# Kernel tuning notes

Measured on AMD Instinct MI355X. Metric: run time of the kernel, lower is better.

Reference implementation:

```python
import jax, jax.numpy as jnp
import numpy as np

# ---- module hyperparameters (from init_kwargs / tracker defaults) ----
D_MODEL = 512
D_HEAD = 512
LAMBDA_0 = 1.0        # A_0 = I / lambda_0
FIXED_LAMBDA = 1.0    # fixed penalty magnitude -> U = sqrt(lambda) * K (then / sqrt(d_head))
STAB_EPS = 1e-6       # InversePenaltyTracker.stabilization_eps
PERIODIC_EPS = 1e-6   # InversePenaltyTracker.periodic_eps
PERIOD = 128          # InversePenaltyTracker.period (periodic re-regularization)
EXPLODE_EPS = 1e-5    # fallback_add_explode coefficient
NORM_THRESH = 1000.0  # explosion detection threshold on Frobenius norms


def setup_inputs() -> dict:
    key = jax.random.key(0)
    ks = jax.random.split(key, 9)
    B, T, d = 8, 2048, D_MODEL
    s = 1.0 / np.sqrt(d)
    f32 = jnp.float32
    return {
        "x": jax.random.normal(ks[0], (B, T, d), f32),
        "Wq": (jax.random.normal(ks[1], (D_HEAD, d), f32) * s),
        "bq": jax.random.normal(ks[2], (D_HEAD,), f32) * 0.02,
        "Wk": (jax.random.normal(ks[3], (D_HEAD, d), f32) * s),
        "bk": jax.random.normal(ks[4], (D_HEAD,), f32) * 0.02,
        "Wv": (jax.random.normal(ks[5], (D_HEAD, d), f32) * s),
        "bv": jax.random.normal(ks[6], (D_HEAD,), f32) * 0.02,
        "Wo": (jax.random.normal(ks[7], (d, D_HEAD), f32) * s),
        "bo": jax.random.normal(ks[8], (d,), f32) * 0.02,
    }


def _vla_forward(x, Wq, bq, Wk, bk, Wv, bv, Wo, bo):
    B, T, _ = x.shape
    d = D_HEAD
    # projections (nn.Linear: x @ W.T + b)
    Q = jnp.einsum('btd,hd->bth', x, Wq) + bq
    K = jnp.einsum('btd,hd->bth', x, Wk) + bk
    V = jnp.einsum('btd,hd->bth', x, Wv) + bv

    # PenaltyBuilder (rank 1, fixed lambda): u_t = sqrt(lambda) * k_t, then / sqrt(d_head)
    U = (jnp.sqrt(jnp.float32(FIXED_LAMBDA)) / jnp.sqrt(jnp.float32(d))) * K
    s_seq = jnp.sum(K * Q, axis=-1)                                   # (B,T)
    Vn = V / (jnp.linalg.norm(V, axis=-1, keepdims=True) + 1e-6)      # (B,T,d)

    I = jnp.eye(d, dtype=jnp.float32)
    A0 = jnp.zeros((B, d, d), jnp.float32) + I / LAMBDA_0
    S0 = jnp.zeros((B, d, d), jnp.float32)

    def step(carry, inp):
        A, S = carry
        q, u, s_t, vn, t = inp  # q,u,vn: (B,d); s_t: (B,); t: scalar int
        # Sherman-Morrison rank-1 inverse update with stabilization
        z = jnp.einsum('bij,bj->bi', A, u)
        dot = jnp.sum(u * z, axis=-1)
        delta = jnp.maximum(1.0 + dot, 1e-6)
        unstable = (jnp.abs(delta) < STAB_EPS) | ~jnp.isfinite(delta)
        safe = jnp.where(unstable, 1.0, delta)
        upd = (z[:, :, None] * z[:, None, :]) / safe[:, None, None]
        A = jnp.where(unstable[:, None, None], A + STAB_EPS * I, A - upd)
        # periodic re-regularization (inv_step = t+1)
        A = jnp.where(((t + 1) % PERIOD) == 0, A + PERIODIC_EPS * I, A)
        # alpha_t = s_t * (A u_t)
        z2 = jnp.einsum('bij,bj->bi', A, u)
        alpha = s_t[:, None] * z2
        # memory update S += v_norm alpha^T
        S = S + vn[:, :, None] * alpha[:, None, :]
        # explosion guard
        Sn = jnp.linalg.norm(S.reshape(S.shape[0], -1), axis=-1)
        An = jnp.linalg.norm(A.reshape(A.shape[0], -1), axis=-1)
        A = jnp.where(((Sn > NORM_THRESH) | (An > NORM_THRESH))[:, None, None],
                      A + EXPLODE_EPS * I, A)
        o = jnp.einsum('bij,bj->bi', S, q)
        return (A, S), o

    xs = (jnp.swapaxes(Q, 0, 1), jnp.swapaxes(U, 0, 1),
          jnp.swapaxes(s_seq, 0, 1), jnp.swapaxes(Vn, 0, 1),
          jnp.arange(T))
    _, O = jax.lax.scan(step, (A0, S0), xs)    # O: (T,B,d)
    O = jnp.swapaxes(O, 0, 1)                  # (B,T,d)
    return jnp.einsum('bth,dh->btd', O, Wo) + bo


def reference(x, Wq, bq, Wk, bk, Wv, bv, Wo, bo):
    return _vla_forward(x, Wq, bq, Wk, bk, Wv, bv, Wo, bo)
```

## Files before the change

kernel.cpp:

```cpp
#include <hip/hip_runtime.h>
#include <hip/hip_bf16.h>

#define BB 8
#define TT 2048
#define DD 512
#define LL 128
#define NC 16
#define ETH 512

typedef unsigned short u16;
typedef unsigned int u32;
typedef __attribute__((ext_vector_type(8))) short bf16x8v;
typedef __attribute__((ext_vector_type(4))) float f32x4v;

__device__ __forceinline__ float bf2f(u32 h) { return __uint_as_float(h << 16); }
__device__ __forceinline__ u16 f2bf(float f) {
    u32 u = __float_as_uint(f);
    u += 0x7fffu + ((u >> 16) & 1u);
    return (u16)(u >> 16);
}
__device__ __forceinline__ float wred64(float v) {
    #pragma unroll
    for (int off = 32; off; off >>= 1) v += __shfl_xor(v, off);
    return v;
}
__device__ __forceinline__ void unpack8(uint4 r, float* f) {
    f[0] = bf2f(r.x & 0xffff); f[1] = bf2f(r.x >> 16);
    f[2] = bf2f(r.y & 0xffff); f[3] = bf2f(r.y >> 16);
    f[4] = bf2f(r.z & 0xffff); f[5] = bf2f(r.z >> 16);
    f[6] = bf2f(r.w & 0xffff); f[7] = bf2f(r.w >> 16);
}

__global__ __launch_bounds__(256)
void f2bf_kernel(const float4* __restrict__ in, ushort4* __restrict__ out, const int n4)
{
    int i = blockIdx.x * 256 + threadIdx.x;
    const int stride = gridDim.x * 256;
    for (; i < n4; i += stride) {
        const float4 v = in[i];
        ushort4 o;
        o.x = f2bf(v.x); o.y = f2bf(v.y); o.z = f2bf(v.z); o.w = f2bf(v.w);
        out[i] = o;
    }
}

__global__ __launch_bounds__(256)
void wconv_kernel(const float4* __restrict__ Wq, const float4* __restrict__ Wk,
                  const float4* __restrict__ Wv, const float4* __restrict__ Wo,
                  ushort4* __restrict__ oq, ushort4* __restrict__ ok,
                  ushort4* __restrict__ ov, ushort4* __restrict__ oo)
{
    const int i = blockIdx.x * 256 + threadIdx.x;
    const int y = blockIdx.y;
    const float4* src = (y == 0) ? Wq : (y == 1) ? Wk : (y == 2) ? Wv : Wo;
    ushort4* dst = (y == 0) ? oq : (y == 1) ? ok : (y == 2) ? ov : oo;
    const float4 v = src[i];
    ushort4 o;
    o.x = f2bf(v.x); o.y = f2bf(v.y); o.z = f2bf(v.z); o.w = f2bf(v.w);
    dst[i] = o;
}

template<int OUT_BF>
__global__ __launch_bounds__(256)
void mfma_gemm(const u16* __restrict__ Abf, const u16* __restrict__ Bbf,
               const float* __restrict__ bias, void* __restrict__ Cout,
               const float outscale)
{
    __shared__ u16 Asm[128 * 64];
    __shared__ u16 Bsm[128 * 64];
    const int tid = threadIdx.x;
    const int wave = tid >> 6, lane = tid & 63;
    const int wm = wave >> 1, wn = wave & 1;
    const int m0 = blockIdx.x * 128, n0 = blockIdx.y * 128;

    f32x4v acc[4][4];
    #pragma unroll
    for (int i = 0; i < 4; ++i)
        #pragma unroll
        for (int j = 0; j < 4; ++j)
            acc[i][j] = (f32x4v){0.f, 0.f, 0.f, 0.f};

    const u16* gsrcA[4];
    const u16* gsrcB[4];
    #pragma unroll
    for (int i = 0; i < 4; ++i) {
        const int idx = i * 256 + tid;
        const int row = idx >> 3, c = idx & 7;
        const int kb = c ^ (row & 7);
        gsrcA[i] = Abf + (size_t)(m0 + row) * 512 + kb * 8;
        gsrcB[i] = Bbf + (size_t)(n0 + row) * 512 + kb * 8;
    }

    for (int k0 = 0; k0 < 512; k0 += 64) {
        __syncthreads();
        #pragma unroll
        for (int i = 0; i < 4; ++i) {
            __builtin_amdgcn_global_load_lds(
                (__attribute__((address_space(1))) void*)(gsrcA[i] + k0),
                (__attribute__((address_space(3))) void*)(Asm + (size_t)(i * 256 + wave * 64) * 8),
                16, 0, 0);
            __builtin_amdgcn_global_load_lds(
                (__attribute__((address_space(1))) void*)(gsrcB[i] + k0),
                (__attribute__((address_space(3))) void*)(Bsm + (size_t)(i * 256 + wave * 64) * 8),
                16, 0, 0);
        }
        asm volatile("s_waitcnt vmcnt(0)" ::: "memory");
        __syncthreads();

        const int l15 = lane & 15, lhi = lane >> 4;
        bf16x8v af[4][2], bfr[4][2];
        #pragma unroll
        for (int mf = 0; mf < 4; ++mf) {
            const int row = wm * 64 + mf * 16 + l15;
            const int sw = (row & 7) << 4;
            #pragma unroll
            for (int ks = 0; ks < 2; ++ks) {
                const int kbyte = ks * 64 + lhi * 16;
                af[mf][ks] = *(const bf16x8v*)((const char*)Asm + row * 128 + (kbyte ^ sw));
            }
        }
        #pragma unroll
        for (int nf = 0; nf < 4; ++nf) {
            const int row = wn * 64 + nf * 16 + l15;
            const int sw = (row & 7) << 4;
            #pragma unroll
            for (int ks = 0; ks < 2; ++ks) {
                const int kbyte = ks * 64 + lhi * 16;
                bfr[nf][ks] = *(const bf16x8v*)((const char*)Bsm + row * 128 + (kbyte ^ sw));
            }
        }
        #pragma unroll
        for (int ks = 0; ks < 2; ++ks)
            #pragma unroll
            for (int mf = 0; mf < 4; ++mf)
                #pragma unroll
                for (int nf = 0; nf < 4; ++nf)
                    acc[mf][nf] = __builtin_amdgcn_mfma_f32_16x16x32_bf16(
                        af[mf][ks], bfr[nf][ks], acc[mf][nf], 0, 0, 0);
    }
    const int l15 = lane & 15, lhi = lane >> 4;
    #pragma unroll
    for (int mf = 0; mf < 4; ++mf) {
        #pragma unroll
        for (int nf = 0; nf < 4; ++nf) {
            const int n = n0 + wn * 64 + nf * 16 + l15;
            const float bsv = bias[n];
            #pragma unroll
            for (int r = 0; r < 4; ++r) {
                const int m = m0 + wm * 64 + mf * 16 + lhi * 4 + r;
                const float val = (acc[mf][nf][r] + bsv) * outscale;
                if (OUT_BF) ((u16*)Cout)[(size_t)m * 512 + n] = f2bf(val);
                else        ((float*)Cout)[(size_t)m * 512 + n] = val;
            }
        }
    }
}

__device__ __forceinline__ void mfk6_body(const u16* __restrict__ Sb,
    const u16* __restrict__ Qt, const u16* __restrict__ AlT,
    const u16* __restrict__ Vnt, float* __restrict__ OBSA,
    float* __restrict__ dsum, const int bz)
{
    __shared__ u16 Ah[128 * 64];
    __shared__ u16 Bh[128 * 64];
    const int tid = threadIdx.x, wave = tid >> 6, lane = tid & 63;
    const int wm = wave >> 1, wn = wave & 1;
    const int m0 = blockIdx.x * 128, n0 = blockIdx.y * 128;

    f32x4v acc[4][4];
    #pragma unroll
    for (int i = 0; i < 4; ++i)
        #pragma unroll
        for (int j = 0; j < 4; ++j)
            acc[i][j] = (f32x4v){0.f, 0.f, 0.f, 0.f};

    const u16* Abase = Sb + (size_t)bz * 262144;
    const u16* Bbase = (n0 == 0) ? (Qt + (size_t)bz * 1048576)
                                 : (AlT + (size_t)bz * 65536);
    const u16* gA[4]; const u16* gB[4];
    #pragma unroll
    for (int i = 0; i < 4; ++i) {
        const int idx = i * 256 + tid, row = idx >> 3, c = idx & 7;
        const int kb = c ^ (row & 7);
        gA[i] = Abase + (size_t)(m0 + row) * 512 + kb * 8;
        gB[i] = Bbase + (size_t)row * 512 + kb * 8;
    }
    for (int k0 = 0; k0 < 512; k0 += 64) {
        __syncthreads();
        #pragma unroll
        for (int i = 0; i < 4; ++i) {
            const int dst = (i * 256 + wave * 64) * 8;
            __builtin_amdgcn_global_load_lds(
                (__attribute__((address_space(1))) void*)(gA[i] + k0),
                (__attribute__((address_space(3))) void*)(Ah + dst), 16, 0, 0);
            __builtin_amdgcn_global_load_lds(
                (__attribute__((address_space(1))) void*)(gB[i] + k0),
                (__attribute__((address_space(3))) void*)(Bh + dst), 16, 0, 0);
        }
        asm volatile("s_waitcnt vmcnt(0)" ::: "memory");
        __syncthreads();

        const int l15 = lane & 15, lhi = lane >> 4;
        bf16x8v af[4][2], bfr[4][2];
        #pragma unroll
        for (int mf = 0; mf < 4; ++mf) {
            const int row = wm * 64 + mf * 16 + l15, sw = (row & 7) << 4;
            #pragma unroll
            for (int ks = 0; ks < 2; ++ks) {
                const int kb2 = (ks * 64 + lhi * 16) ^ sw;
                af[mf][ks] = *(const bf16x8v*)((const char*)Ah + row * 128 + kb2);
            }
        }
        #pragma unroll
        for (int nf = 0; nf < 4; ++nf) {
            const int row = wn * 64 + nf * 16 + l15, sw = (row & 7) << 4;
            #pragma unroll
            for (int ks = 0; ks < 2; ++ks) {
                const int kb2 = (ks * 64 + lhi * 16) ^ sw;
                bfr[nf][ks] = *(const bf16x8v*)((const char*)Bh + row * 128 + kb2);
            }
        }
        #pragma unroll
        for (int ks = 0; ks < 2; ++ks)
            #pragma unroll
            for (int mf = 0; mf < 4; ++mf)
                #pragma unroll
                for (int nf = 0; nf < 4; ++nf)
                    acc[mf][nf] = __builtin_amdgcn_mfma_f32_16x16x32_bf16(
                        af[mf][ks], bfr[nf][ks], acc[mf][nf], 0, 0, 0);
    }
    const int l15 = lane & 15, lhi = lane >> 4;
    float* C = OBSA + (size_t)bz * 131072;
    #pragma unroll
    for (int mf = 0; mf < 4; ++mf)
        #pragma unroll
        for (int nf = 0; nf < 4; ++nf) {
            const int n = n0 + wn * 64 + nf * 16 + l15;
            #pragma unroll
            for (int r = 0; r < 4; ++r) {
                const int m = m0 + wm * 64 + mf * 16 + lhi * 4 + r;
                C[(size_t)m * 256 + n] = acc[mf][nf][r];
            }
        }
    if (n0 == 128) {
        const u16* Vn = Vnt + (size_t)bz * 1048576;
        #pragma unroll
        for (int nf = 0; nf < 4; ++nf) {
            const int n = n0 + wn * 64 + nf * 16 + l15;
            const int i2 = n - 128;
            float part = 0.f;
            #pragma unroll
            for (int mf = 0; mf < 4; ++mf) {
                const int m = m0 + wm * 64 + mf * 16 + lhi * 4;
                const ushort4 vr = *(const ushort4*)(Vn + (size_t)i2 * 512 + m);
                part += bf2f(vr.x) * acc[mf][nf][0] + bf2f(vr.y) * acc[mf][nf][1]
                      + bf2f(vr.z) * acc[mf][nf][2] + bf2f(vr.w) * acc[mf][nf][3];
            }
            part += __shfl_xor(part, 16);
            part += __shfl_xor(part, 32);
            if (lhi == 0) atomicAdd(dsum + bz * 128 + i2, part);
        }
    }
}

__global__ __launch_bounds__(256)
void prep_kernel(const u16* __restrict__ Qb, const u16* __restrict__ Ub,
                 u16* __restrict__ Vb, float* __restrict__ sseq)
{
    const int lane = threadIdx.x & 63, wid = threadIdx.x >> 6;
    const int row = blockIdx.x * 4 + wid;
    const size_t base = (size_t)row * DD;
    const uint4 qr = *(const uint4*)(Qb + base + lane * 8);
    const uint4 ur = *(const uint4*)(Ub + base + lane * 8);
    const uint4 vr = *(const uint4*)(Vb + base + lane * 8);
    float q[8], u[8], v[8];
    unpack8(qr, q); unpack8(ur, u); unpack8(vr, v);
    float sd = 0.f, nv = 0.f;
    #pragma unroll
    for (int e = 0; e < 8; ++e) { sd = fmaf(q[e], u[e], sd); nv = fmaf(v[e], v[e], nv); }
    #pragma unroll
    for (int off = 32; off; off >>= 1) { sd += __shfl_xor(sd, off); nv += __shfl_xor(nv, off); }
    if (lane == 0) sseq[row] = sd * 22.627416997969522f;
    const float inv = 1.f / (sqrtf(nv) + 1e-6f);
    uint4 o;
    o.x = (u32)f2bf(v[0] * inv) | ((u32)f2bf(v[1] * inv) << 16);
    o.y = (u32)f2bf(v[2] * inv) | ((u32)f2bf(v[3] * inv) << 16);
    o.z = (u32)f2bf(v[4] * inv) | ((u32)f2bf(v[5] * inv) << 16);
    o.w = (u32)f2bf(v[6] * inv) | ((u32)f2bf(v[7] * inv) << 16);
    *(uint4*)(Vb + base + lane * 8) = o;
}

__global__ __launch_bounds__(256)
void init_kernel(float4* __restrict__ A4, float4* __restrict__ S4,
                 ushort4* __restrict__ Sbf4,
                 float* __restrict__ SnSq, float* __restrict__ AnAcc)
{
    const int gtid = blockIdx.x * 256 + threadIdx.x;
    const int N4 = BB * DD * DD / 4;
    const ushort4 z4 = {0, 0, 0, 0};
    for (int idx = gtid; idx < N4; idx += gridDim.x * 256) {
        const int e0 = idx << 2;
        const int r = (e0 >> 9) & 511;
        const int c = e0 & 511;
        float4 v;
        v.x = (c + 0 == r) ? 1.f : 0.f;
        v.y = (c + 1 == r) ? 1.f : 0.f;
        v.z = (c + 2 == r) ? 1.f : 0.f;
        v.w = (c + 3 == r) ? 1.f : 0.f;
        A4[idx] = v;
        S4[idx] = make_float4(0.f, 0.f, 0.f, 0.f);
        Sbf4[idx] = z4;
    }
    if (gtid < BB) { SnSq[gtid] = 0.f; AnAcc[gtid] = 512.f; }
}

struct GP {
    int alay, blay, epi;
    const void* Ap; const void* Bp;
    void* Cp; float* Cio;
    const float* gdiag; float* anacc;
    const float* invdp; const float* cap; const float* cbp;
    const u16* Ulastp; float* Zsp; float* Alphap;
    u16* albt; u16* sbf;
    int lda, ldb, ldc, K;
    long sA, sB, sC, sCio;
};

__device__ __forceinline__ void gemm_body(const GP& p, const int bz) {
    __shared__ __align__(16) float As[32][68];
    __shared__ __align__(16) float Bs[32][68];
    const int m0 = blockIdx.x * 64, n0 = blockIdx.y * 64;
    const int tid = threadIdx.x, tx = tid & 15, ty = tid >> 4;
    float acc[4][4] = {};
    for (int k0 = 0; k0 < p.K; k0 += 32) {
        if (p.alay == 0) {
            const float* A = (const float*)p.Ap + (size_t)bz * p.sA;
            #pragma unroll
            for (int h = 0; h < 2; ++h) {
                const int g = tid + h * 256, m = g >> 3, k4 = (g & 7) * 4;
                const float4 r = *(const float4*)(A + (size_t)(m0 + m) * p.lda + k0 + k4);
                As[k4][m] = r.x; As[k4+1][m] = r.y; As[k4+2][m] = r.z; As[k4+3][m] = r.w;
            }
        } else if (p.alay == 2) {
            const u16* A = (const u16*)p.Ap + (size_t)bz * p.sA;
            #pragma unroll
            for (int h = 0; h < 2; ++h) {
                const int g = tid + h * 256, m = g >> 3, k4 = (g & 7) * 4;
                const ushort4 r = *(const ushort4*)(A + (size_t)(m0 + m) * p.lda + k0 + k4);
                As[k4][m]=bf2f(r.x); As[k4+1][m]=bf2f(r.y); As[k4+2][m]=bf2f(r.z); As[k4+3][m]=bf2f(r.w);
            }
        } else if (p.alay == 1 || p.alay == 4) {
            const float* A = (const float*)p.Ap + (size_t)bz * p.sA;
            #pragma unroll
            for (int h = 0; h < 2; ++h) {
                const int g = tid + h * 256, k = g >> 4, m4 = (g & 15) * 4;
                float4 r = *(const float4*)(A + (size_t)(k0 + k) * p.lda + m0 + m4);
                if (p.alay == 4) {
                    const int kg = k0 + k, mg = m0 + m4;
                    if (kg > mg + 0) r.x = 0.f;
                    if (kg > mg + 1) r.y = 0.f;
                    if (kg > mg + 2) r.z = 0.f;
                    if (kg > mg + 3) r.w = 0.f;
                }
                As[k][m4] = r.x; As[k][m4+1] = r.y; As[k][m4+2] = r.z; As[k][m4+3] = r.w;
            }
        } else {
            const u16* A = (const u16*)p.Ap + (size_t)bz * p.sA;
            #pragma unroll
            for (int h = 0; h < 2; ++h) {
                const int g = tid + h * 256, k = g >> 4, m4 = (g & 15) * 4;
                const ushort4 r = *(const ushort4*)(A + (size_t)(k0 + k) * p.lda + m0 + m4);
                As[k][m4]=bf2f(r.x); As[k][m4+1]=bf2f(r.y); As[k][m4+2]=bf2f(r.z); As[k][m4+3]=bf2f(r.w);
            }
        }
        if (p.blay == 0) {
            const float* B = (const float*)p.Bp + (size_t)bz * p.sB;
            #pragma unroll
            for (int h = 0; h < 2; ++h) {
                const int g = tid + h * 256, k = g >> 4, n4 = (g & 15) * 4;
                const float4 r = *(const float4*)(B + (size_t)(k0 + k) * p.ldb + n0 + n4);
                Bs[k][n4] = r.x; Bs[k][n4+1] = r.y; Bs[k][n4+2] = r.z; Bs[k][n4+3] = r.w;
            }
        } else if (p.blay == 2) {
            const u16* B = (const u16*)p.Bp + (size_t)bz * p.sB;
            #pragma unroll
            for (int h = 0; h < 2; ++h) {
                const int g = tid + h * 256, k = g >> 4, n4 = (g & 15) * 4;
                const ushort4 r = *(const ushort4*)(B + (size_t)(k0 + k) * p.ldb + n0 + n4);
                Bs[k][n4]=bf2f(r.x); Bs[k][n4+1]=bf2f(r.y); Bs[k][n4+2]=bf2f(r.z); Bs[k][n4+3]=bf2f(r.w);
            }
        } else if (p.blay == 1) {
            const float* B = (const float*)p.Bp + (size_t)bz * p.sB;
            #pragma unroll
            for (int h = 0; h < 2; ++h) {
                const int g = tid + h * 256, n = g >> 3, k4 = (g & 7) * 4;
                const float4 r = *(const float4*)(B + (size_t)(n0 + n) * p.ldb + k0 + k4);
                Bs[k4][n] = r.x; Bs[k4+1][n] = r.y; Bs[k4+2][n] = r.z; Bs[k4+3][n] = r.w;
            }
        } else {
            const u16* B = (const u16*)p.Bp + (size_t)bz * p.sB;
            #pragma unroll
            for (int h = 0; h < 2; ++h) {
                const int g = tid + h * 256, n = g >> 3, k4 = (g & 7) * 4;
                const ushort4 r = *(const ushort4*)(B + (size_t)(n0 + n) * p.ldb + k0 + k4);
                Bs[k4][n]=bf2f(r.x); Bs[k4+1][n]=bf2f(r.y); Bs[k4+2][n]=bf2f(r.z); Bs[k4+3][n]=bf2f(r.w);
            }
        }
        __syncthreads();
        #pragma unroll
        for (int kk = 0; kk < 32; ++kk) {
            const float4 xa = *(const float4*)&As[kk][ty * 4];
            const float4 wb = *(const float4*)&Bs[kk][tx * 4];
            const float xv[4] = {xa.x, xa.y, xa.z, xa.w};
            const float wv[4] = {wb.x, wb.y, wb.z, wb.w};
            #pragma unroll
            for (int i = 0; i < 4; ++i)
                #pragma unroll
                for (int j = 0; j < 4; ++j)
                    acc[i][j] = fmaf(xv[i], wv[j], acc[i][j]);
        }
        __syncthreads();
    }
    const int mb = m0 + ty * 4, nb = n0 + tx * 4;
    if (p.epi == 0) {
        float* C = (float*)p.Cp + (size_t)bz * p.sC;
        #pragma unroll
        for (int i = 0; i < 4; ++i)
            #pragma unroll
            for (int j = 0; j < 4; ++j)
                C[(size_t)(mb + i) * p.ldc + nb + j] = acc[i][j];
    } else if (p.epi == 1) {
        float* C = p.Cio + (size_t)bz * p.sCio;
        const float gd = p.gdiag[bz];
        float v2 = 0.f;
        #pragma unroll
        for (int i = 0; i < 4; ++i)
            #pragma unroll
            for (int j = 0; j < 4; ++j) {
                const size_t idx = (size_t)(mb + i) * p.ldc + nb + j;
                float v = C[idx] - acc[i][j] + ((mb + i) == (nb + j) ? gd : 0.f);
                C[idx] = v;
                v2 = fmaf(v, v, v2);
            }
        v2 = wred64(v2);
        if ((tid & 63) == 0) atomicAdd(p.anacc + bz, v2);
    } else if (p.epi == 2) {
        float* C = p.Cio + (size_t)bz * p.sCio;
        u16* SB = p.sbf + (size_t)bz * p.sCio;
        #pragma unroll
        for (int i = 0; i < 4; ++i)
            #pragma unroll
            for (int j = 0; j < 4; ++j) {
                const size_t idx = (size_t)(mb + i) * p.ldc + nb + j;
                const float v = C[idx] + acc[i][j];
                C[idx] = v;
                SB[idx] = f2bf(v);
            }
    } else if (p.epi == 3) {
        u16* O = (u16*)p.Cp + (size_t)bz * p.sC;
        const float* OB = p.Cio + (size_t)bz * p.sCio;
        #pragma unroll
        for (int i = 0; i < 4; ++i)
            #pragma unroll
            for (int j = 0; j < 4; ++j)
                O[(size_t)(mb + i) * p.ldc + nb + j] =
                    f2bf(acc[i][j] + OB[(size_t)(nb + j) * 256 + mb + i]);
    } else {
        float* Zb  = (float*)p.Cp + (size_t)bz * 65536;
        float* Zsb = p.Zsp + (size_t)bz * 65536;
        float* Apb = p.Alphap + (size_t)bz * 65536;
        #pragma unroll
        for (int j = 0; j < 4; ++j) {
            const int n = nb + j;
            const float iv = p.invdp[bz * 128 + n];
            const float cav = p.cap[bz * 128 + n];
            const float cbv = p.cbp[bz * 128 + n];
            #pragma unroll
            for (int i = 0; i < 4; ++i) {
                const int m = mb + i;
                const float z = acc[i][j];
                const size_t o = (size_t)m * 128 + n;
                Zb[o] = z;
                Zsb[o] = z * iv;
                float a = z * cav;
                if (cbv != 0.f) a = fmaf(cbv, bf2f(p.Ulastp[(size_t)bz * 1048576 + m]), a);
                Apb[o] = a;
                p.albt[(size_t)bz * 65536 + (size_t)n * 512 + m] = f2bf(a);
            }
        }
    }
}

__global__ __launch_bounds__(256) void gemmx(GP p) { gemm_body(p, blockIdx.z); }

__global__ __launch_bounds__(256)
void lvl5_kernel(const u16* Sb, const u16* AlT, const float* Alpha,
                 const u16* Qt, const u16* Vnt,
                 float* P, float* Ga, float* Gv, float* OBSA, float* dsum)
{
    const int z = blockIdx.z;
    if (z < 8) {
        mfk6_body(Sb, Qt, AlT, Vnt, OBSA, dsum, z);
        return;
    }
    if (blockIdx.x >= 2 || blockIdx.y >= 2) return;
    const int zz = z - 8, b = zz / 3, j = zz - b * 3;
    GP p{};
    p.K = 512; p.epi = 0; p.ldc = 128; p.sC = 16384;
    if (j == 0) {
        p.alay = 1; p.Ap = Alpha; p.lda = 128; p.sA = 65536;
        p.blay = 3; p.Bp = Qt; p.ldb = 512; p.sB = 1048576; p.Cp = P;
    } else if (j == 1) {
        p.alay = 1; p.Ap = Alpha; p.lda = 128; p.sA = 65536;
        p.blay = 0; p.Bp = Alpha; p.ldb = 128; p.sB = 65536; p.Cp = Ga;
    } else {
        p.alay = 2; p.Ap = Vnt; p.lda = 512; p.sA = 1048576;
        p.blay = 3; p.Bp = Vnt; p.ldb = 512; p.sB = 1048576; p.Cp = Gv;
    }
    gemm_body(p, b);
}

__global__ __launch_bounds__(256)
void lvl7_kernel(const float* P, const u16* Vnt, u16* Obt, const float* OBSA,
                 const float* Alpha, const float* Zs, const float* Z,
                 float* S, u16* Sbf, float* A, const float* gdiag, float* AnAcc)
{
    const int z = blockIdx.z;
    GP p{};
    if (z < 8) {
        p.alay = 0; p.Ap = Zs; p.lda = 128; p.sA = 65536;
        p.blay = 1; p.Bp = Z; p.ldb = 128; p.sB = 65536;
        p.epi = 1; p.Cio = A; p.sCio = 262144; p.ldc = 512;
        p.gdiag = gdiag; p.anacc = AnAcc; p.K = 128;
        gemm_body(p, z);
    } else if (z < 16) {
        p.alay = 3; p.Ap = Vnt; p.lda = 512; p.sA = 1048576;
        p.blay = 1; p.Bp = Alpha; p.ldb = 128; p.sB = 65536;
        p.epi = 2; p.Cio = S; p.sbf = Sbf; p.sCio = 262144; p.ldc = 512; p.K = 128;
        gemm_body(p, z - 8);
    } else {
        if (blockIdx.x >= 2) return;
        p.alay = 4; p.Ap = P; p.lda = 128; p.sA = 16384;
        p.blay = 2; p.Bp = Vnt; p.ldb = 512; p.sB = 1048576;
        p.epi = 3; p.Cp = Obt; p.ldc = 512; p.sC = 1048576;
        p.Cio = (float*)OBSA; p.sCio = 131072; p.K = 128;
        gemm_body(p, z - 16);
    }
}

__global__ __launch_bounds__(512)
void elim_kernel(const float* __restrict__ G, float* __restrict__ Tg,
                 const float* __restrict__ sseq, float* __restrict__ invd,
                 float* __restrict__ ca, float* __restrict__ cb,
                 float* __restrict__ dsum_g, const int t0)
{
    const int b = blockIdx.x, tid = threadIdx.x, lane = tid & 63, wave = tid >> 6;
    __shared__ __align__(16) float E[128][132];
    __shared__ __align__(16) float Cs[128][132];
    __shared__ __align__(16) float LpT[8][132];
    __shared__ __align__(16) float SpT[8][132];
    __shared__ float Msc[8][8][9];
    __shared__ float del[128];
    float (*Tm)[132] = E;

    {
        const float4* Gb = (const float4*)(G + (size_t)b * 16384);
        for (int idx = tid; idx < 4096; idx += ETH) {
            const int r = idx >> 5, c4 = idx & 31;
            ((float4*)&E[r][0])[c4] = Gb[idx];
        }
    }
    if (tid < 128) dsum_g[b * 128 + tid] = 0.f;
    __syncthreads();

    for (int p = 0; p < 16; ++p) {
        const int pc0 = p * 8;
        if (wave == 0) {
            float pr0[8], pr1[8];
            #pragma unroll
            for (int j = 0; j < 8; ++j) {
                pr0[j] = E[pc0 + j][lane];
                pr1[j] = E[pc0 + j][64 + lane];
            }
            float dl[8];
            const bool hi = (pc0 >= 64);
            #pragma unroll
            for (int j = 0; j < 8; ++j) {
                const int t = pc0 + j;
                const int pl = t & 63;
                float prow[8];
                #pragma unroll
                for (int c = 0; c < 8; ++c) {
                    const float v0 = __shfl(pr0[c], pl);
                    const float v1 = __shfl(pr1[c], pl);
                    prow[c] = hi ? v1 : v0;
                }
                const float d = fmaxf(1.f + prow[j], 1e-6f);
                dl[j] = d;
                const float inv = 1.f / d;
                if (lane > t) {
                    const float coef = pr0[j] * inv;
                    #pragma unroll
                    for (int c = j + 1; c < 8; ++c) pr0[c] = fmaf(-coef, prow[c], pr0[c]);
                }
                if (lane + 64 > t) {
                    const float coef = pr1[j] * inv;
                    #pragma unroll
                    for (int c = j + 1; c < 8; ++c) pr1[c] = fmaf(-coef, prow[c], pr1[c]);
                }
            }
            #pragma unroll
            for (int j = 0; j < 8; ++j) {
                const float idj = 1.f / dl[j];
                const int t = pc0 + j;
                {
                    const bool below = (lane > t);
                    const float y = below ? pr0[j] : 0.f;
                    const float l = y * idj;
                    LpT[j][lane] = l; SpT[j][lane] = y; Cs[t][lane] = l;
                }
                {
                    const int r = lane + 64;
                    const bool below = (r > t);
                    const float y = below ? pr1[j] : 0.f;
                    const float l = y * idj;
                    LpT[j][r] = l; SpT[j][r] = y; Cs[t][r] = l;
                }
            }
            if (lane < 8) del[pc0 + lane] = dl[lane];
        }
        __syncthreads();
        const int r0b = pc0 + 8;
        if (r0b < 128) {
            const int nrows = 128 - r0b;
            const int c40 = r0b >> 2, nc4 = 32 - c40;
            for (int idx = tid; idx < nrows * nc4; idx += ETH) {
                const int rr = idx / nc4, cc = idx - rr * nc4;
                const int r = r0b + rr, c4 = c40 + cc;
                float4 e = ((float4*)&E[r][0])[c4];
                #pragma unroll
                for (int j = 0; j < 8; ++j) {
                    const float lv = LpT[j][r];
                    const float4 sv = ((const float4*)&SpT[j][0])[c4];
                    e.x = fmaf(-lv, sv.x, e.x);
                    e.y = fmaf(-lv, sv.y, e.y);
                    e.z = fmaf(-lv, sv.z, e.z);
                    e.w = fmaf(-lv, sv.w, e.w);
                }
                ((float4*)&E[r][0])[c4] = e;
            }
        }
        __syncthreads();
    }

    for (int idx = tid; idx < 4224; idx += ETH)
        ((float4*)&Tm[0][0])[idx] = make_float4(0.f, 0.f, 0.f, 0.f);
    __syncthreads();
    if (tid < 128) Tm[tid][tid] = 1.f;
    __syncthreads();
    {
        const int g = tid >> 3, c = tid & 7;
        if (g < 16) {
            for (int r2 = c - 1; r2 >= 0; --r2) {
                float s = 0.f;
                for (int kk = r2 + 1; kk <= c; ++kk)
                    s = fmaf(Cs[8 * g + r2][8 * g + kk],
                             (kk == c) ? 1.f : Tm[8 * g + kk][8 * g + c], s);
                Tm[8 * g + r2][8 * g + c] = -s;
            }
        }
    }
    __syncthreads();
    const int rr8 = lane >> 3, cc8 = lane & 7;
    #pragma unroll
    for (int which = 0; which < 2; ++which) {
        const int j = which ? (15 - wave) : wave;
        for (int i = j - 1; i >= 0; --i) {
            float m = 0.f;
            for (int l = i + 1; l <= j; ++l) {
                #pragma unroll
                for (int kk = 0; kk < 8; ++kk)
                    m = fmaf(Cs[8 * i + rr8][8 * l + kk], Tm[8 * l + kk][8 * j + cc8], m);
            }
            Msc[wave][rr8][cc8] = m;
            float s = 0.f;
            #pragma unroll
            for (int kk = 0; kk < 8; ++kk)
                s = fmaf(Tm[8 * i + rr8][8 * i + kk], Msc[wave][kk][cc8], s);
            Tm[8 * i + rr8][8 * j + cc8] = -s;
        }
    }
    __syncthreads();
    {
        float4* Tgb = (float4*)(Tg + (size_t)b * 16384);
        for (int idx = tid; idx < 4096; idx += ETH) {
            const int r = idx >> 5, c4 = idx & 31;
            Tgb[idx] = ((const float4*)&Tm[r][0])[c4];
        }
    }
    if (tid < 128) {
        const float d = del[tid];
        const float s = sseq[(size_t)b * TT + t0 + tid];
        invd[b * 128 + tid] = 1.f / d;
        ca[b * 128 + tid] = s / d;
        cb[b * 128 + tid] = (tid == 127) ? s * 1e-6f : 0.f;
    }
}

__global__ __launch_bounds__(256)
void guard_kernel(const float* __restrict__ dsum_g, const float* __restrict__ Ga,
                  const float* __restrict__ Gv, float* __restrict__ SnSq,
                  float* __restrict__ AnAcc, float* __restrict__ gdiag)
{
    const int b = blockIdx.x, tid = threadIdx.x;
    __shared__ float rpart[256], dsh[128], mdia[128];
    const int t = tid & 127, half = tid >> 7;
    const float* gv = Gv + (size_t)b * 16384 + t * 128;
    const float* ga = Ga + (size_t)b * 16384 + t * 128;
    float rs = 0.f;
    for (int j = half; j < t; j += 2) rs = fmaf(gv[j], ga[j], rs);
    rpart[tid] = rs;
    if (half == 0) { dsh[t] = dsum_g[b * 128 + t]; mdia[t] = gv[t] * ga[t]; }
    __syncthreads();
    if (tid == 0) {
        const float An2 = AnAcc[b];
        float Sn2 = SnSq[b], D = 0.f, T = 0.f;
        int ng = 0;
        for (int t2 = 0; t2 < 128; ++t2) {
            D += dsh[t2];
            T += mdia[t2] + 2.f * (rpart[t2] + rpart[t2 + 128]);
            const float sn2 = Sn2 + 2.f * D + T;
            if (sn2 > 1e6f || An2 > 1e6f) ++ng;
        }
        SnSq[b] = Sn2 + 2.f * D + T;
        gdiag[b] = 1e-6f + (float)ng * 1e-5f;
        AnAcc[b] = 0.f;
    }
}

extern "C" void kernel_launch(void* const* d_in, const int* in_sizes, int n_in,
                              void* d_out, int out_size, void* d_ws, size_t ws_size,
                              hipStream_t stream)
{
    const float* x  = (const float*)d_in[0];
    const float* Wq = (const float*)d_in[1];
    const float* bq = (const float*)d_in[2];
    const float* Wk = (const float*)d_in[3];
    const float* bk = (const float*)d_in[4];
    const float* Wv = (const float*)d_in[5];
    const float* bv = (const float*)d_in[6];
    const float* Wo = (const float*)d_in[7];
    const float* bo = (const float*)d_in[8];

    char* ws = (char*)d_ws;
    u16* Qb    = (u16*)(ws);
    u16* Ub    = (u16*)(ws + (16ull << 20));
    u16* Vnb   = (u16*)(ws + (32ull << 20));
    u16* Ob    = (u16*)(ws + (48ull << 20));
    u16* x_bf  = Ob;
    float* A    = (float*)(ws + (64ull << 20));
    float* S    = (float*)(ws + (72ull << 20));
    float* Wm   = (float*)(ws + (80ull << 20));
    float* Z    = (float*)(ws + (82ull << 20));
    float* Zs   = (float*)(ws + (84ull << 20));
    float* Alpha= (float*)(ws + (86ull << 20));
    float* OBSA = (float*)(ws + (88ull << 20));
    float* G    = (float*)(ws + (92ull << 20));
    float* Tg   = (float*)(ws + (92ull << 20) + (512ull << 10));
    float* P    = (float*)(ws + (93ull << 20));
    float* Ga   = (float*)(ws + (93ull << 20) + (512ull << 10));
    float* Gv   = (float*)(ws + (94ull << 20));
    float* invd = (float*)(ws + (94ull << 20) + (512ull << 10));
    float* ca   = (float*)(ws + (94ull << 20) + (516ull << 10));
    float* cb   = (float*)(ws + (94ull << 20) + (520ull << 10));
    float* sseq = (float*)(ws + (94ull << 20) + (528ull << 10));
    float* SnSq = (float*)(ws + (94ull << 20) + (600ull << 10));
    float* AnAcc= (float*)(ws + (94ull << 20) + (600ull << 10) + 64);
    float* gdiag= (float*)(ws + (94ull << 20) + (600ull << 10) + 128);
    float* dsum = (float*)(ws + (94ull << 20) + (604ull << 10));
    u16* Wq_bf = (u16*)(ws + (95ull << 20));
    u16* Wk_bf = (u16*)(ws + (95ull << 20) + (512ull << 10));
    u16* Wv_bf = (u16*)(ws + (96ull << 20));
    u16* Wo_bf = (u16*)(ws + (96ull << 20) + (512ull << 10));
    u16* S_bf  = (u16*)(ws + (97ull << 20));
    u16* AlT   = (u16*)(ws + (101ull << 20));

    f2bf_kernel<<<2048, 256, 0, stream>>>((const float4*)x, (ushort4*)x_bf, 2097152);
    wconv_kernel<<<dim3(256, 4), 256, 0, stream>>>(
        (const float4*)Wq, (const float4*)Wk, (const float4*)Wv, (const float4*)Wo,
        (ushort4*)Wq_bf, (ushort4*)Wk_bf, (ushort4*)Wv_bf, (ushort4*)Wo_bf);

    mfma_gemm<1><<<dim3(128, 4), 256, 0, stream>>>(x_bf, Wq_bf, bq, Qb, 1.f);
    mfma_gemm<1><<<dim3(128, 4), 256, 0, stream>>>(x_bf, Wk_bf, bk, Ub, 0.04419417382415922f);
    mfma_gemm<1><<<dim3(128, 4), 256, 0, stream>>>(x_bf, Wv_bf, bv, Vnb, 1.f);
    prep_kernel<<<4096, 256, 0, stream>>>(Qb, Ub, Vnb, sseq);
    init_kernel<<<2048, 256, 0, stream>>>((float4*)A, (float4*)S, (ushort4*)S_bf, SnSq, AnAcc);

    for (int c = 0; c < NC; ++c) {
        const int t0 = c * LL;
        const u16* Ut = Ub + (size_t)t0 * 512;
        const u16* Qt = Qb + (size_t)t0 * 512;
        const u16* Vt = Vnb + (size_t)t0 * 512;
        GP p1{}; p1.alay = 0; p1.Ap = A; p1.lda = 512; p1.sA = 262144;
        p1.blay = 3; p1.Bp = Ut; p1.ldb = 512; p1.sB = 1048576;
        p1.epi = 0; p1.Cp = Wm; p1.ldc = 128; p1.sC = 65536; p1.K = 512;
        gemmx<<<dim3(8, 2, 8), 256, 0, stream>>>(p1);
        GP p2{}; p2.alay = 2; p2.Ap = Ut; p2.lda = 512; p2.sA = 1048576;
        p2.blay = 0; p2.Bp = Wm; p2.ldb = 128; p2.sB = 65536;
        p2.epi = 0; p2.Cp = G; p2.ldc = 128; p2.sC = 16384; p2.K = 512;
        gemmx<<<dim3(2, 2, 8), 256, 0, stream>>>(p2);
        elim_kernel<<<8, 512, 0, stream>>>(G, Tg, sseq, invd, ca, cb, dsum, t0);
        GP p4{}; p4.alay = 0; p4.Ap = Wm; p4.lda = 128; p4.sA = 65536;
        p4.blay = 0; p4.Bp = Tg; p4.ldb = 128; p4.sB = 16384;
        p4.epi = 4; p4.Cp = Z; p4.Zsp = Zs; p4.Alphap = Alpha; p4.albt = AlT;
        p4.invdp = invd; p4.cap = ca; p4.cbp = cb;
        p4.Ulastp = Ub + (size_t)(t0 + 127) * 512;
        p4.K = 128; p4.ldc = 128; p4.sC = 65536;
        gemmx<<<dim3(8, 2, 8), 256, 0, stream>>>(p4);
        lvl5_kernel<<<dim3(4, 2, 32), 256, 0, stream>>>(S_bf, AlT, Alpha, Qt, Vt,
            P, Ga, Gv, OBSA, dsum);
        guard_kernel<<<8, 256, 0, stream>>>(dsum, Ga, Gv, SnSq, AnAcc, gdiag);
        lvl7_kernel<<<dim3(8, 8, 24), 256, 0, stream>>>(P, Vt, Ob + (size_t)t0 * 512, OBSA,
            Alpha, Zs, Z, S, S_bf, A, gdiag, AnAcc);
    }
    mfma_gemm<0><<<dim3(128, 4), 256, 0, stream>>>(Ob, Wo_bf, bo, d_out, 1.f);
}
```

Measured before the change: 3.662 ms.

## Overlap alpha-independent GEMMs (S·Q, Vn Gram) with the serial elimination kernel

Work that does not depend on alpha moves out of the level-5 kernel and into the same launch as the single-block-per-batch elimination kernel. That work is the S_bf×Q half of the OBSA product and the Vn Gram matrix Gv, computed by new dedicated bodies. The idle CUs can then do it while elimination runs. The elimination kernel now uses a carved-up dynamic-style shared buffer of about 143KB, and every block in the launch allocates it, which may limit co-residency. lvl5 keeps only the alpha-dependent parts.

```diff
diff --git a/kernel.cpp b/kernel.cpp
--- a/kernel.cpp
+++ b/kernel.cpp
@@ -261,6 +261,132 @@
             if (lhi == 0) atomicAdd(dsum + bz * 128 + i2, part);
         }
     }
+}
+
+__device__ __forceinline__ void mfk6q8_body(char* smemc,
+    const u16* __restrict__ Sb, const u16* __restrict__ Qt,
+    float* __restrict__ OBSA, const int bz)
+{
+    u16* Ah = (u16*)smemc;
+    u16* Bh = (u16*)(smemc + 16384);
+    const int tid = threadIdx.x, wave = tid >> 6, lane = tid & 63;
+    const int wm = wave >> 1, wn = wave & 1;
+    const int m0 = blockIdx.x * 128;
+
+    f32x4v acc[2][4];
+    #pragma unroll
+    for (int i = 0; i < 2; ++i)
+        #pragma unroll
+        for (int j = 0; j < 4; ++j)
+            acc[i][j] = (f32x4v){0.f, 0.f, 0.f, 0.f};
+
+    const u16* Abase = Sb + (size_t)bz * 262144;
+    const u16* Bbase = Qt + (size_t)bz * 1048576;
+    const u16* gA[2]; const u16* gB[2];
+    #pragma unroll
+    for (int i = 0; i < 2; ++i) {
+        const int idx = i * 512 + tid, row = idx >> 3, c = idx & 7;
+        const int kb = c ^ (row & 7);
+        gA[i] = Abase + (size_t)(m0 + row) * 512 + kb * 8;
+        gB[i] = Bbase + (size_t)row * 512 + kb * 8;
+    }
+    for (int k0 = 0; k0 < 512; k0 += 64) {
+        __syncthreads();
+        #pragma unroll
+        for (int i = 0; i < 2; ++i) {
+            const int dst = (i * 512 + wave * 64) * 8;
+            __builtin_amdgcn_global_load_lds(
+                (__attribute__((address_space(1))) void*)(gA[i] + k0),
+                (__attribute__((address_space(3))) void*)(Ah + dst), 16, 0, 0);
+            __builtin_amdgcn_global_load_lds(
+                (__attribute__((address_space(1))) void*)(gB[i] + k0),
+                (__attribute__((address_space(3))) void*)(Bh + dst), 16, 0, 0);
+        }
+        asm volatile("s_waitcnt vmcnt(0)" ::: "memory");
+        __syncthreads();
+
+        const int l15 = lane & 15, lhi = lane >> 4;
+        bf16x8v af[2][2], bfr[4][2];
+        #pragma unroll
+        for (int mf = 0; mf < 2; ++mf) {
+            const int row = wm * 32 + mf * 16 + l15, sw = (row & 7) << 4;
+            #pragma unroll
+            for (int ks = 0; ks < 2; ++ks) {
+                const int kb2 = (ks * 64 + lhi * 16) ^ sw;
+                af[mf][ks] = *(const bf16x8v*)((const char*)Ah + row * 128 + kb2);
+            }
+        }
+        #pragma unroll
+        for (int nf = 0; nf < 4; ++nf) {
+            const int row = wn * 64 + nf * 16 + l15, sw = (row & 7) << 4;
+            #pragma unroll
+            for (int ks = 0; ks < 2; ++ks) {
+                const int kb2 = (ks * 64 + lhi * 16) ^ sw;
+                bfr[nf][ks] = *(const bf16x8v*)((const char*)Bh + row * 128 + kb2);
+            }
+        }
+        #pragma unroll
+        for (int ks = 0; ks < 2; ++ks)
+            #pragma unroll
+            for (int mf = 0; mf < 2; ++mf)
+                #pragma unroll
+                for (int nf = 0; nf < 4; ++nf)
+                    acc[mf][nf] = __builtin_amdgcn_mfma_f32_16x16x32_bf16(
+                        af[mf][ks], bfr[nf][ks], acc[mf][nf], 0, 0, 0);
+    }
+    const int l15 = lane & 15, lhi = lane >> 4;
+    float* C = OBSA + (size_t)bz * 131072;
+    #pragma unroll
+    for (int mf = 0; mf < 2; ++mf)
+        #pragma unroll
+        for (int nf = 0; nf < 4; ++nf) {
+            const int n = wn * 64 + nf * 16 + l15;
+            #pragma unroll
+            for (int r = 0; r < 4; ++r) {
+                const int m = m0 + wm * 32 + mf * 16 + lhi * 4 + r;
+                C[(size_t)m * 256 + n] = acc[mf][nf][r];
+            }
+        }
+}
+
+__device__ __forceinline__ void gv512_body(char* smemc, const u16* __restrict__ Vnt,
+    float* __restrict__ Gv, const int b)
+{
+    float (*As)[68] = (float(*)[68])smemc;
+    float (*Bs)[68] = (float(*)[68])(smemc + 8704);
+    const int tid = threadIdx.x;
+    const int m0 = blockIdx.x * 64, n0 = blockIdx.y * 64;
+    const u16* Vn = Vnt + (size_t)b * 1048576;
+    const int tx = tid & 15, ty = tid >> 4;
+    float acc[2][4] = {};
+    for (int k0 = 0; k0 < 512; k0 += 32) {
+        const int m = tid >> 3, k4 = (tid & 7) * 4;
+        const ushort4 ra = *(const ushort4*)(Vn + (size_t)(m0 + m) * 512 + k0 + k4);
+        As[k4][m]=bf2f(ra.x); As[k4+1][m]=bf2f(ra.y); As[k4+2][m]=bf2f(ra.z); As[k4+3][m]=bf2f(ra.w);
+        const ushort4 rb = *(const ushort4*)(Vn + (size_t)(n0 + m) * 512 + k0 + k4);
+        Bs[k4][m]=bf2f(rb.x); Bs[k4+1][m]=bf2f(rb.y); Bs[k4+2][m]=bf2f(rb.z); Bs[k4+3][m]=bf2f(rb.w);
+        __syncthreads();
+        #pragma unroll
+        for (int kk = 0; kk < 32; ++kk) {
+            const float a0 = As[kk][ty * 2], a1 = As[kk][ty * 2 + 1];
+            const float4 bv = *(const float4*)&Bs[kk][tx * 4];
+            acc[0][0] = fmaf(a0, bv.x, acc[0][0]);
+            acc[0][1] = fmaf(a0, bv.y, acc[0][1]);
+            acc[0][2] = fmaf(a0, bv.z, acc[0][2]);
+            acc[0][3] = fmaf(a0, bv.w, acc[0][3]);
+            acc[1][0] = fmaf(a1, bv.x, acc[1][0]);
+            acc[1][1] = fmaf(a1, bv.y, acc[1][1]);
+            acc[1][2] = fmaf(a1, bv.z, acc[1][2]);
+            acc[1][3] = fmaf(a1, bv.w, acc[1][3]);
+        }
+        __syncthreads();
+    }
+    float* G = Gv + (size_t)b * 16384;
+    #pragma unroll
+    for (int i = 0; i < 2; ++i)
+        #pragma unroll
+        for (int j = 0; j < 4; ++j)
+            G[(size_t)(m0 + ty * 2 + i) * 128 + n0 + tx * 4 + j] = acc[i][j];
 }
 
 __global__ __launch_bounds__(256)
@@ -493,74 +619,36 @@
 
 __global__ __launch_bounds__(256) void gemmx(GP p) { gemm_body(p, blockIdx.z); }
 
-__global__ __launch_bounds__(256)
-void lvl5_kernel(const u16* Sb, const u16* AlT, const float* Alpha,
-                 const u16* Qt, const u16* Vnt,
-                 float* P, float* Ga, float* Gv, float* OBSA, float* dsum)
-{
-    const int z = blockIdx.z;
-    if (z < 8) {
-        mfk6_body(Sb, Qt, AlT, Vnt, OBSA, dsum, z);
-        return;
-    }
-    if (blockIdx.x >= 2 || blockIdx.y >= 2) return;
-    const int zz = z - 8, b = zz / 3, j = zz - b * 3;
-    GP p{};
-    p.K = 512; p.epi = 0; p.ldc = 128; p.sC = 16384;
-    if (j == 0) {
-        p.alay = 1; p.Ap = Alpha; p.lda = 128; p.sA = 65536;
-        p.blay = 3; p.Bp = Qt; p.ldb = 512; p.sB = 1048576; p.Cp = P;
-    } else if (j == 1) {
-        p.alay = 1; p.Ap = Alpha; p.lda = 128; p.sA = 65536;
-        p.blay = 0; p.Bp = Alpha; p.ldb = 128; p.sB = 65536; p.Cp = Ga;
-    } else {
-        p.alay = 2; p.Ap = Vnt; p.lda = 512; p.sA = 1048576;
-        p.blay = 3; p.Bp = Vnt; p.ldb = 512; p.sB = 1048576; p.Cp = Gv;
-    }
-    gemm_body(p, b);
-}
-
-__global__ __launch_bounds__(256)
-void lvl7_kernel(const float* P, const u16* Vnt, u16* Obt, const float* OBSA,
-                 const float* Alpha, const float* Zs, const float* Z,
-                 float* S, u16* Sbf, float* A, const float* gdiag, float* AnAcc)
-{
-    const int z = blockIdx.z;
-    GP p{};
-    if (z < 8) {
-        p.alay = 0; p.Ap = Zs; p.lda = 128; p.sA = 65536;
-        p.blay = 1; p.Bp = Z; p.ldb = 128; p.sB = 65536;
-        p.epi = 1; p.Cio = A; p.sCio = 262144; p.ldc = 512;
-        p.gdiag = gdiag; p.anacc = AnAcc; p.K = 128;
-        gemm_body(p, z);
-    } else if (z < 16) {
-        p.alay = 3; p.Ap = Vnt; p.lda = 512; p.sA = 1048576;
-        p.blay = 1; p.Bp = Alpha; p.ldb = 128; p.sB = 65536;
-        p.epi = 2; p.Cio = S; p.sbf = Sbf; p.sCio = 262144; p.ldc = 512; p.K = 128;
-        gemm_body(p, z - 8);
-    } else {
-        if (blockIdx.x >= 2) return;
-        p.alay = 4; p.Ap = P; p.lda = 128; p.sA = 16384;
-        p.blay = 2; p.Bp = Vnt; p.ldb = 512; p.sB = 1048576;
-        p.epi = 3; p.Cp = Obt; p.ldc = 512; p.sC = 1048576;
-        p.Cio = (float*)OBSA; p.sCio = 131072; p.K = 128;
-        gemm_body(p, z - 16);
-    }
-}
-
 __global__ __launch_bounds__(512)
-void elim_kernel(const float* __restrict__ G, float* __restrict__ Tg,
+void lvl3_kernel(const float* __restrict__ G, float* __restrict__ Tg,
                  const float* __restrict__ sseq, float* __restrict__ invd,
                  float* __restrict__ ca, float* __restrict__ cb,
-                 float* __restrict__ dsum_g, const int t0)
-{
-    const int b = blockIdx.x, tid = threadIdx.x, lane = tid & 63, wave = tid >> 6;
-    __shared__ __align__(16) float E[128][132];
-    __shared__ __align__(16) float Cs[128][132];
-    __shared__ __align__(16) float LpT[8][132];
-    __shared__ __align__(16) float SpT[8][132];
-    __shared__ float Msc[8][8][9];
-    __shared__ float del[128];
+                 float* __restrict__ dsum_g,
+                 const u16* __restrict__ Vnt, const u16* __restrict__ Sb,
+                 const u16* __restrict__ Qt, float* __restrict__ Gv,
+                 float* __restrict__ OBSA, const int t0)
+{
+    __shared__ __align__(16) char smem[146432];
+    const int z = blockIdx.z;
+    if (z >= 16) {
+        if (blockIdx.y != 0) return;
+        mfk6q8_body(smem, Sb, Qt, OBSA, z - 16);
+        return;
+    }
+    if (z >= 8) {
+        if (blockIdx.x >= 2 || blockIdx.y >= 2) return;
+        gv512_body(smem, Vnt, Gv, z - 8);
+        return;
+    }
+    if (blockIdx.x != 0 || blockIdx.y != 0) return;
+
+    const int b = z, tid = threadIdx.x, lane = tid & 63, wave = tid >> 6;
+    float (*E)[132]    = (float(*)[132])smem;
+    float (*Cs)[132]   = (float(*)[132])(smem + 67584);
+    float (*LpT)[132]  = (float(*)[132])(smem + 135168);
+    float (*SpT)[132]  = (float(*)[132])(smem + 139392);
+    float (*Msc)[8][9] = (float(*)[8][9])(smem + 143616);
+    float* del         = (float*)(smem + 145920);
     float (*Tm)[132] = E;
 
     {
@@ -704,6 +792,59 @@
         invd[b * 128 + tid] = 1.f / d;
         ca[b * 128 + tid] = s / d;
         cb[b * 128 + tid] = (tid == 127) ? s * 1e-6f : 0.f;
+    }
+}
+
+__global__ __launch_bounds__(256)
+void lvl5b_kernel(const u16* Sb, const u16* AlT, const float* Alpha,
+                  const u16* Qt, const u16* Vnt,
+                  float* P, float* Ga, float* OBSA, float* dsum)
+{
+    const int z = blockIdx.z;
+    if (z < 8) {
+        if (blockIdx.y != 1) return;
+        mfk6_body(Sb, Qt, AlT, Vnt, OBSA, dsum, z);
+        return;
+    }
+    if (blockIdx.x >= 2 || blockIdx.y >= 2) return;
+    GP p{};
+    p.K = 512; p.epi = 0; p.ldc = 128; p.sC = 16384;
+    if (z < 16) {
+        p.alay = 1; p.Ap = Alpha; p.lda = 128; p.sA = 65536;
+        p.blay = 3; p.Bp = Qt; p.ldb = 512; p.sB = 1048576; p.Cp = P;
+        gemm_body(p, z - 8);
+    } else {
+        p.alay = 1; p.Ap = Alpha; p.lda = 128; p.sA = 65536;
+        p.blay = 0; p.Bp = Alpha; p.ldb = 128; p.sB = 65536; p.Cp = Ga;
+        gemm_body(p, z - 16);
+    }
+}
+
+__global__ __launch_bounds__(256)
+void lvl7_kernel(const float* P, const u16* Vnt, u16* Obt, const float* OBSA,
+                 const float* Alpha, const float* Zs, const float* Z,
+                 float* S, u16* Sbf, float* A, const float* gdiag, float* AnAcc)
+{
+    const int z = blockIdx.z;
+    GP p{};
+    if (z < 8) {
+        p.alay = 0; p.Ap = Zs; p.lda = 128; p.sA = 65536;
+        p.blay = 1; p.Bp = Z; p.ldb = 128; p.sB = 65536;
+        p.epi = 1; p.Cio = A; p.sCio = 262144; p.ldc = 512;
+        p.gdiag = gdiag; p.anacc = AnAcc; p.K = 128;
+        gemm_body(p, z);
+    } else if (z < 16) {
+        p.alay = 3; p.Ap = Vnt; p.lda = 512; p.sA = 1048576;
+        p.blay = 1; p.Bp = Alpha; p.ldb = 128; p.sB = 65536;
+        p.epi = 2; p.Cio = S; p.sbf = Sbf; p.sCio = 262144; p.ldc = 512; p.K = 128;
+        gemm_body(p, z - 8);
+    } else {
+        if (blockIdx.x >= 2) return;
+        p.alay = 4; p.Ap = P; p.lda = 128; p.sA = 16384;
+        p.blay = 2; p.Bp = Vnt; p.ldb = 512; p.sB = 1048576;
+        p.epi = 3; p.Cp = Obt; p.ldc = 512; p.sC = 1048576;
+        p.Cio = (float*)OBSA; p.sCio = 131072; p.K = 128;
+        gemm_body(p, z - 16);
     }
 }
 
@@ -809,7 +950,8 @@
         p2.blay = 0; p2.Bp = Wm; p2.ldb = 128; p2.sB = 65536;
         p2.epi = 0; p2.Cp = G; p2.ldc = 128; p2.sC = 16384; p2.K = 512;
         gemmx<<<dim3(2, 2, 8), 256, 0, stream>>>(p2);
-        elim_kernel<<<8, 512, 0, stream>>>(G, Tg, sseq, invd, ca, cb, dsum, t0);
+        lvl3_kernel<<<dim3(4, 2, 24), 512, 0, stream>>>(G, Tg, sseq, invd, ca, cb,
+            dsum, Vt, S_bf, Qt, Gv, OBSA, t0);
         GP p4{}; p4.alay = 0; p4.Ap = Wm; p4.lda = 128; p4.sA = 65536;
         p4.blay = 0; p4.Bp = Tg; p4.ldb = 128; p4.sB = 16384;
         p4.epi = 4; p4.Cp = Z; p4.Zsp = Zs; p4.Alphap = Alpha; p4.albt = AlT;
@@ -817,8 +959,8 @@
         p4.Ulastp = Ub + (size_t)(t0 + 127) * 512;
         p4.K = 128; p4.ldc = 128; p4.sC = 65536;
         gemmx<<<dim3(8, 2, 8), 256, 0, stream>>>(p4);
-        lvl5_kernel<<<dim3(4, 2, 32), 256, 0, stream>>>(S_bf, AlT, Alpha, Qt, Vt,
-            P, Ga, Gv, OBSA, dsum);
+        lvl5b_kernel<<<dim3(4, 2, 24), 256, 0, stream>>>(S_bf, AlT, Alpha, Qt, Vt,
+            P, Ga, OBSA, dsum);
         guard_kernel<<<8, 256, 0, stream>>>(dsum, Ga, Gv, SnSq, AnAcc, gdiag);
         lvl7_kernel<<<dim3(8, 8, 24), 256, 0, stream>>>(P, Vt, Ob + (size_t)t0 * 512, OBSA,
             Alpha, Zs, Z, S, S_bf, A, gdiag, AnAcc);
```

New measurement: 3.835 ms. 4.7% more time.
